# Performance work log

Hardware: AMD Instinct MI355X
Metric: run time of the kernel (lower is better)

Reference implementation:

```python
import jax, jax.numpy as jnp
import numpy as np

D_MODEL = 2048
N_HEADS = 16
D_K = D_MODEL // N_HEADS
NB_FEAT = 8  # ceil(ln(2048))
BLOCK_H = 1
BLOCK_W = 1
EPS = 1e-6


def setup_inputs() -> dict:
    key = jax.random.key(0)
    ks = jax.random.split(key, 8)
    B, S = 2, 4096
    q = jax.random.normal(ks[0], (B, S, D_MODEL), dtype=jnp.float32)
    k = jax.random.normal(ks[1], (B, S, D_MODEL), dtype=jnp.float32)
    v = jax.random.normal(ks[2], (B, S, D_MODEL), dtype=jnp.float32)
    # torch Linear weights [out, in]
    w_q = jax.random.normal(ks[3], (D_MODEL, D_MODEL), dtype=jnp.float32) / np.sqrt(D_MODEL)
    w_k = jax.random.normal(ks[4], (D_MODEL, D_MODEL), dtype=jnp.float32) / np.sqrt(D_MODEL)
    w_v = jax.random.normal(ks[5], (D_MODEL, D_MODEL), dtype=jnp.float32) / np.sqrt(D_MODEL)
    w_o = jax.random.normal(ks[6], (D_MODEL, D_MODEL), dtype=jnp.float32) / np.sqrt(D_MODEL)
    omega = jax.random.normal(ks[7], (NB_FEAT, D_K), dtype=jnp.float32) / np.sqrt(D_K)
    return {"q": q, "k": k, "v": v, "w_q": w_q, "w_k": w_k, "w_v": w_v, "w_o": w_o, "omega": omega}


def _kernel(x):
    # kernel_type == 'exp'
    return jnp.exp(-0.5 * x * x)


def reference(q, k, v, w_q, w_k, w_v, w_o, omega):
    B, Sq, D = q.shape
    Sk = k.shape[1]
    # projections (torch Linear: x @ W.T), split heads -> [B, S, H, d_k]
    qh = (q @ w_q.T).reshape(B, Sq, N_HEADS, D_K)
    kh = (k @ w_k.T).reshape(B, Sk, N_HEADS, D_K)
    vh = (v @ w_v.T).reshape(B, Sk, N_HEADS, D_K)
    # random-feature maps -> [B, S, H, nb]
    q_prime = _kernel(jnp.einsum('bshd,nd->bshn', qh, omega))
    k_prime = _kernel(jnp.einsum('bshd,nd->bshn', kh, omega))
    q_prime = q_prime / (q_prime.sum(-1, keepdims=True) + EPS)
    k_prime = k_prime / (k_prime.sum(-1, keepdims=True) + EPS)
    # causal prefix sums along sequence
    K_cum = jnp.cumsum(k_prime, axis=1)                                   # [B,S,H,nb]
    KV_cum = jnp.cumsum(k_prime[..., None] * vh[..., None, :], axis=1)    # [B,S,H,nb,d_k]
    # blockwise causal key selection
    q_idx = jnp.arange(Sq)
    key_idx = jnp.minimum((q_idx // BLOCK_H + 1) * BLOCK_W - 1, Sk - 1)   # [Sq]
    K_sel = K_cum[:, key_idx]    # [B,Sq,H,nb]
    KV_sel = KV_cum[:, key_idx]  # [B,Sq,H,nb,d_k]
    numerator = jnp.einsum('bshn,bshnd->bshd', q_prime, KV_sel)
    denominator = jnp.sum(q_prime * K_sel, axis=-1, keepdims=True)
    out = numerator / (denominator + EPS)
    out = out.reshape(B, Sq, D)
    return out @ w_o.T
```

## Files before the change

### kernel.cpp

```cpp
#include <hip/hip_runtime.h>
#include <hip/hip_bf16.h>
#include <cstdint>

#define B_SZ 2
#define S_LEN 4096
#define R_TOT 8192
#define DM 2048
#define NH 16
#define DK 128
#define NFEAT 8
#define CHUNK 128
#define NCHUNK 32
#define KSPL 512
#define EPSF 1e-6f

typedef short bf16x8_t __attribute__((ext_vector_type(8)));
typedef float f32x4_t __attribute__((ext_vector_type(4)));

__device__ __forceinline__ ushort f2bf(float f) {
  uint32_t u = __float_as_uint(f);
  u += 0x7FFF + ((u >> 16) & 1);
  return (ushort)(u >> 16);
}
__device__ __forceinline__ float bf2f(ushort u) {
  return __uint_as_float(((uint32_t)u) << 16);
}

__global__ __launch_bounds__(256) void prep_kernel(const float* __restrict__ v,
                                                   const float* __restrict__ w_v,
                                                   const float* __restrict__ w_o,
                                                   const float* __restrict__ w_q,
                                                   const float* __restrict__ w_k,
                                                   const float* __restrict__ omega,
                                                   ushort* __restrict__ xb,
                                                   ushort* __restrict__ wvb,
                                                   ushort* __restrict__ wob,
                                                   ushort* __restrict__ oqb,
                                                   ushort* __restrict__ okb) {
  const int bid = blockIdx.x;
  if (bid < 16384) {
    const int i = bid * 256 + threadIdx.x;
    float4 f = reinterpret_cast<const float4*>(v)[i];
    ushort4 o;
    o.x = f2bf(f.x); o.y = f2bf(f.y); o.z = f2bf(f.z); o.w = f2bf(f.w);
    reinterpret_cast<ushort4*>(xb)[i] = o;
  } else if (bid < 24576) {
    const int wb = bid - 16384;
    const float* src = (wb >= 4096) ? w_o : w_v;
    ushort* dst = (wb >= 4096) ? wob : wvb;
    const int i = (wb & 4095) * 256 + threadIdx.x;
    float4 f = reinterpret_cast<const float4*>(src)[i];
    ushort4 o;
    o.x = f2bf(f.x); o.y = f2bf(f.y); o.z = f2bf(f.z); o.w = f2bf(f.w);
    reinterpret_cast<ushort4*>(dst)[i] = o;
  } else {
    __shared__ float som[NFEAT * DK];
    const int fb = bid - 24576;
    const int z = fb >> 7, h = (fb >> 3) & 15, jb = fb & 7;
    const float* W = z ? w_k : w_q;
    ushort* O = z ? okb : oqb;
    const int j = jb * 256 + threadIdx.x;
    for (int i = threadIdx.x; i < NFEAT * DK; i += 256) som[i] = omega[i];
    __syncthreads();
    float acc[NFEAT] = {0.f, 0.f, 0.f, 0.f, 0.f, 0.f, 0.f, 0.f};
    for (int d = 0; d < DK; d++) {
      const float w = W[(size_t)(h * DK + d) * DM + j];
#pragma unroll
      for (int n = 0; n < NFEAT; n++) acc[n] += w * som[n * DK + d];
    }
#pragma unroll
    for (int n = 0; n < NFEAT; n++) O[(size_t)(h * NFEAT + n) * DM + j] = f2bf(acc[n]);
  }
}

#define MFMA_BLK(mb, A0_, A1_, A2_, A3_, B0_, B1_, B2_, B3_)                                  \
  acc[mb + 0][0] = __builtin_amdgcn_mfma_f32_16x16x32_bf16(A0_, B0_, acc[mb + 0][0], 0, 0, 0); \
  acc[mb + 1][0] = __builtin_amdgcn_mfma_f32_16x16x32_bf16(A1_, B0_, acc[mb + 1][0], 0, 0, 0); \
  acc[mb + 2][0] = __builtin_amdgcn_mfma_f32_16x16x32_bf16(A2_, B0_, acc[mb + 2][0], 0, 0, 0); \
  acc[mb + 3][0] = __builtin_amdgcn_mfma_f32_16x16x32_bf16(A3_, B0_, acc[mb + 3][0], 0, 0, 0); \
  acc[mb + 0][1] = __builtin_amdgcn_mfma_f32_16x16x32_bf16(A0_, B1_, acc[mb + 0][1], 0, 0, 0); \
  acc[mb + 1][1] = __builtin_amdgcn_mfma_f32_16x16x32_bf16(A1_, B1_, acc[mb + 1][1], 0, 0, 0); \
  acc[mb + 2][1] = __builtin_amdgcn_mfma_f32_16x16x32_bf16(A2_, B1_, acc[mb + 2][1], 0, 0, 0); \
  acc[mb + 3][1] = __builtin_amdgcn_mfma_f32_16x16x32_bf16(A3_, B1_, acc[mb + 3][1], 0, 0, 0); \
  acc[mb + 0][2] = __builtin_amdgcn_mfma_f32_16x16x32_bf16(A0_, B2_, acc[mb + 0][2], 0, 0, 0); \
  acc[mb + 1][2] = __builtin_amdgcn_mfma_f32_16x16x32_bf16(A1_, B2_, acc[mb + 1][2], 0, 0, 0); \
  acc[mb + 2][2] = __builtin_amdgcn_mfma_f32_16x16x32_bf16(A2_, B2_, acc[mb + 2][2], 0, 0, 0); \
  acc[mb + 3][2] = __builtin_amdgcn_mfma_f32_16x16x32_bf16(A3_, B2_, acc[mb + 3][2], 0, 0, 0); \
  acc[mb + 0][3] = __builtin_amdgcn_mfma_f32_16x16x32_bf16(A0_, B3_, acc[mb + 0][3], 0, 0, 0); \
  acc[mb + 1][3] = __builtin_amdgcn_mfma_f32_16x16x32_bf16(A1_, B3_, acc[mb + 1][3], 0, 0, 0); \
  acc[mb + 2][3] = __builtin_amdgcn_mfma_f32_16x16x32_bf16(A2_, B3_, acc[mb + 2][3], 0, 0, 0); \
  acc[mb + 3][3] = __builtin_amdgcn_mfma_f32_16x16x32_bf16(A3_, B3_, acc[mb + 3][3], 0, 0, 0);

template<int BF16OUT>
__global__ __launch_bounds__(512, 1) void gemm256(const ushort* __restrict__ A,
                                                  const ushort* __restrict__ Bm,
                                                  void* __restrict__ Cv,
                                                  int M, int N, int K) {
  __shared__ ushort lds[8 * 8192];
  const int tid = threadIdx.x;
  const int wave = tid >> 6, lane = tid & 63;
  const int wm = wave >> 2, wn = wave & 3;
  const int NKT = K >> 6;

  const int nb = N >> 8;
  const int cpx = gridDim.x >> 3;
  const int swz = (blockIdx.x & 7) * cpx + (blockIdx.x >> 3);
  const int bx = swz % nb, by = swz / nb;
  const int m0 = by * 256, n0 = bx * 256;

  auto stage = [&](int bufi, int ab, int kh, int kt, const ushort* G, int r0) {
    ushort* Lr = lds + (((bufi << 1) | ab) << 1 | kh) * 8192;
#pragma unroll
    for (int j = 0; j < 2; j++) {
      const int c = j * 512 + wave * 64 + lane;
      const int row = c >> 2, slot = c & 3;
      const int ss = slot ^ ((row >> 1) & 3);
      const ushort* g = G + (size_t)(r0 + row) * K + kt * 64 + kh * 32 + ss * 8;
      __builtin_amdgcn_global_load_lds(
          (const __attribute__((address_space(1))) void*)g,
          (__attribute__((address_space(3))) void*)(Lr + (j * 512 + wave * 64) * 8), 16, 0, 0);
    }
  };
  auto rdA = [&](int bufi, int kh, int m) -> bf16x8_t {
    const int row = wm * 128 + m * 16 + (lane & 15);
    const int slot = (lane >> 4) ^ ((row >> 1) & 3);
    return *reinterpret_cast<const bf16x8_t*>(lds + ((bufi << 2) | kh) * 8192 + row * 32 + slot * 8);
  };
  auto rdB = [&](int bufi, int kh, int nf) -> bf16x8_t {
    const int row = wn * 64 + nf * 16 + (lane & 15);
    const int slot = (lane >> 4) ^ ((row >> 1) & 3);
    return *reinterpret_cast<const bf16x8_t*>(lds + (((bufi << 1) | 1) << 1 | kh) * 8192 + row * 32 + slot * 8);
  };

  f32x4_t acc[8][4];
#pragma unroll
  for (int m = 0; m < 8; m++)
#pragma unroll
    for (int nf = 0; nf < 4; nf++) acc[m][nf] = (f32x4_t){0.f, 0.f, 0.f, 0.f};

  stage(0, 0, 0, 0, A, m0);  stage(0, 1, 0, 0, Bm, n0);
  stage(0, 0, 1, 0, A, m0);  stage(0, 1, 1, 0, Bm, n0);
  stage(1, 0, 0, 1, A, m0);  stage(1, 1, 0, 1, Bm, n0);
  asm volatile("s_waitcnt vmcnt(8)" ::: "memory");
  __builtin_amdgcn_s_barrier();
  __builtin_amdgcn_sched_barrier(0);

  bf16x8_t pA0 = rdA(0, 0, 0), pA1 = rdA(0, 0, 1), pA2 = rdA(0, 0, 2), pA3 = rdA(0, 0, 3);
  bf16x8_t B00 = rdB(0, 0, 0), B01 = rdB(0, 0, 1), B02 = rdB(0, 0, 2), B03 = rdB(0, 0, 3);
  bf16x8_t qA0, qA1, qA2, qA3, B10, B11, B12, B13;

  for (int t = 0; t < NKT; t++) {
    const int buf = t & 1;
    const int t1 = (t + 1 < NKT) ? t + 1 : NKT - 1;
    const int t2 = (t + 2 < NKT) ? t + 2 : NKT - 1;

    qA0 = rdA(buf, 0, 4); qA1 = rdA(buf, 0, 5); qA2 = rdA(buf, 0, 6); qA3 = rdA(buf, 0, 7);
    stage(buf ^ 1, 0, 1, t1, A, m0);
    __builtin_amdgcn_s_setprio(1);
    MFMA_BLK(0, pA0, pA1, pA2, pA3, B00, B01, B02, B03)
    __builtin_amdgcn_s_setprio(0);
    asm volatile("s_waitcnt vmcnt(6)" ::: "memory");
    __builtin_amdgcn_s_barrier();
    __builtin_amdgcn_sched_barrier(0);

    pA0 = rdA(buf, 1, 0); pA1 = rdA(buf, 1, 1); pA2 = rdA(buf, 1, 2); pA3 = rdA(buf, 1, 3);
    B10 = rdB(buf, 1, 0); B11 = rdB(buf, 1, 1); B12 = rdB(buf, 1, 2); B13 = rdB(buf, 1, 3);
    stage(buf ^ 1, 1, 1, t1, Bm, n0);
    __builtin_amdgcn_s_setprio(1);
    MFMA_BLK(4, qA0, qA1, qA2, qA3, B00, B01, B02, B03)
    __builtin_amdgcn_s_setprio(0);
    __builtin_amdgcn_s_barrier();
    __builtin_amdgcn_sched_barrier(0);

    qA0 = rdA(buf, 1, 4); qA1 = rdA(buf, 1, 5); qA2 = rdA(buf, 1, 6); qA3 = rdA(buf, 1, 7);
    stage(buf, 0, 0, t2, A, m0);
    __builtin_amdgcn_s_setprio(1);
    MFMA_BLK(0, pA0, pA1, pA2, pA3, B10, B11, B12, B13)
    __builtin_amdgcn_s_setprio(0);
    asm volatile("s_waitcnt vmcnt(6)" ::: "memory");
    __builtin_amdgcn_s_barrier();
    __builtin_amdgcn_sched_barrier(0);

    pA0 = rdA(buf ^ 1, 0, 0); pA1 = rdA(buf ^ 1, 0, 1); pA2 = rdA(buf ^ 1, 0, 2); pA3 = rdA(buf ^ 1, 0, 3);
    B00 = rdB(buf ^ 1, 0, 0); B01 = rdB(buf ^ 1, 0, 1); B02 = rdB(buf ^ 1, 0, 2); B03 = rdB(buf ^ 1, 0, 3);
    stage(buf, 1, 0, t2, Bm, n0);
    __builtin_amdgcn_s_setprio(1);
    MFMA_BLK(4, qA0, qA1, qA2, qA3, B10, B11, B12, B13)
    __builtin_amdgcn_s_setprio(0);
    __builtin_amdgcn_s_barrier();
    __builtin_amdgcn_sched_barrier(0);
  }
  asm volatile("s_waitcnt vmcnt(0)" ::: "memory");

#pragma unroll
  for (int m = 0; m < 8; m++) {
    const int rb = m0 + wm * 128 + m * 16 + (lane >> 4) * 4;
#pragma unroll
    for (int nf = 0; nf < 4; nf++) {
      const int col = n0 + wn * 64 + nf * 16 + (lane & 15);
#pragma unroll
      for (int r = 0; r < 4; r++) {
        const float val = acc[m][nf][r];
        if (BF16OUT)
          ((ushort*)Cv)[(size_t)(rb + r) * N + col] = f2bf(val);
        else
          ((float*)Cv)[(size_t)(rb + r) * N + col] = val;
      }
    }
  }
}

__global__ __launch_bounds__(256) void gemm_thin2(const float* __restrict__ qin,
                                                  const float* __restrict__ kin,
                                                  const ushort* __restrict__ oqb,
                                                  const ushort* __restrict__ okb,
                                                  float* __restrict__ P) {
  __shared__ ushort lds_a[128 * 32];
  __shared__ ushort lds_b[128 * 32];
  const int which = blockIdx.z;
  const float* A = which ? kin : qin;
  const ushort* Bm = which ? okb : oqb;
  const int t = threadIdx.x;
  const int wave = t >> 6, lane = t & 63;
  const int spl = blockIdx.x;
  const int m0 = blockIdx.y * 128;
  const int kb = spl * KSPL;
  const int wm = wave >> 1, wn = wave & 1;

  f32x4_t acc[4][4];
#pragma unroll
  for (int i = 0; i < 4; i++)
#pragma unroll
    for (int j = 0; j < 4; j++) acc[i][j] = (f32x4_t){0.f, 0.f, 0.f, 0.f};

  const int srow = lane >> 2;
  const int skoff = (lane & 3) * 8;

  for (int k0 = kb; k0 < kb + KSPL; k0 += 32) {
#pragma unroll
    for (int j = 0; j < 2; j++) {
      const int g = j * 256 + t;
      const int row = g >> 2, slot = g & 3;
      const float4* gp = reinterpret_cast<const float4*>(A + (size_t)(m0 + row) * DM + k0 + slot * 8);
      const float4 f0 = gp[0], f1 = gp[1];
      union { ushort u[8]; bf16x8_t v; } pk;
      pk.u[0] = f2bf(f0.x); pk.u[1] = f2bf(f0.y); pk.u[2] = f2bf(f0.z); pk.u[3] = f2bf(f0.w);
      pk.u[4] = f2bf(f1.x); pk.u[5] = f2bf(f1.y); pk.u[6] = f2bf(f1.z); pk.u[7] = f2bf(f1.w);
      *reinterpret_cast<bf16x8_t*>(lds_a + row * 32 + slot * 8) = pk.v;
    }
#pragma unroll
    for (int i = 0; i < 2; i++) {
      const int rgrp = i * 4 + wave;
      const int row = rgrp * 16 + srow;
      const ushort* gb = Bm + (size_t)row * DM + (k0 + skoff);
      __builtin_amdgcn_global_load_lds(
          (const __attribute__((address_space(1))) void*)gb,
          (__attribute__((address_space(3))) void*)(lds_b + rgrp * 512), 16, 0, 0);
    }
    __syncthreads();
    bf16x8_t af[4], bfr[4];
#pragma unroll
    for (int i = 0; i < 4; i++) {
      af[i]  = *reinterpret_cast<const bf16x8_t*>(
          lds_a + (wm * 64 + i * 16 + (lane & 15)) * 32 + (lane >> 4) * 8);
      bfr[i] = *reinterpret_cast<const bf16x8_t*>(
          lds_b + (wn * 64 + i * 16 + (lane & 15)) * 32 + (lane >> 4) * 8);
    }
#pragma unroll
    for (int i = 0; i < 4; i++)
#pragma unroll
      for (int j = 0; j < 4; j++)
        acc[i][j] = __builtin_amdgcn_mfma_f32_16x16x32_bf16(af[i], bfr[j], acc[i][j], 0, 0, 0);
    __syncthreads();
  }

  float* Pp = P + (size_t)which * (4ull * R_TOT * 128) + (size_t)spl * ((size_t)R_TOT * 128);
#pragma unroll
  for (int i = 0; i < 4; i++) {
    const int rb = m0 + wm * 64 + i * 16 + (lane >> 4) * 4;
#pragma unroll
    for (int j = 0; j < 4; j++) {
      const int col = wn * 64 + j * 16 + (lane & 15);
#pragma unroll
      for (int r = 0; r < 4; r++)
        Pp[(size_t)(rb + r) * 128 + col] = acc[i][j][r];
    }
  }
}

__global__ __launch_bounds__(256) void feat2x2(const float* __restrict__ P,
                                               float* __restrict__ qf,
                                               float* __restrict__ kf) {
  const int which = blockIdx.y;
  const float* Pb = P + (size_t)which * (4ull * R_TOT * 128);
  float* F = which ? kf : qf;
  const int g = blockIdx.x * 256 + threadIdx.x;
  const int row = g >> 4, h = g & 15;
  float4 a = {0.f, 0.f, 0.f, 0.f}, c = {0.f, 0.f, 0.f, 0.f};
#pragma unroll
  for (int s = 0; s < 4; s++) {
    const float4* xp = reinterpret_cast<const float4*>(
        Pb + (size_t)s * ((size_t)R_TOT * 128) + (size_t)row * 128 + h * NFEAT);
    const float4 u = xp[0], w = xp[1];
    a.x += u.x; a.y += u.y; a.z += u.z; a.w += u.w;
    c.x += w.x; c.y += w.y; c.z += w.z; c.w += w.w;
  }
  float x[8] = {a.x, a.y, a.z, a.w, c.x, c.y, c.z, c.w};
  float f[8], s = 0.f;
#pragma unroll
  for (int n = 0; n < 8; n++) { f[n] = __expf(-0.5f * x[n] * x[n]); s += f[n]; }
  const float inv = 1.f / (s + EPSF);
  const int b = row >> 12, sidx = row & 4095;
  float* out = F + ((size_t)(h * 2 + b) * 4096 + sidx) * 8;
  float4 o0 = {f[0] * inv, f[1] * inv, f[2] * inv, f[3] * inv};
  float4 o1 = {f[4] * inv, f[5] * inv, f[6] * inv, f[7] * inv};
  reinterpret_cast<float4*>(out)[0] = o0;
  reinterpret_cast<float4*>(out)[1] = o1;
}

__global__ __launch_bounds__(128) void chunk_sum_kernel(const float* __restrict__ KF,
                                                        const ushort* __restrict__ VH,
                                                        float* __restrict__ CKV,
                                                        float* __restrict__ CK) {
  const int cid = blockIdx.x;
  const int c = cid & 31, bh = cid >> 5, b = bh >> 4, h = bh & 15;
  const int d = threadIdx.x;
  __shared__ float s_kf[CHUNK * 8];
  const size_t fbase = ((size_t)(h * 2 + b) * 4096 + (size_t)c * CHUNK) * 8;
  {
    float4 a0 = *reinterpret_cast<const float4*>(KF + fbase + d * 8);
    float4 a1 = *reinterpret_cast<const float4*>(KF + fbase + d * 8 + 4);
    *reinterpret_cast<float4*>(s_kf + d * 8) = a0;
    *reinterpret_cast<float4*>(s_kf + d * 8 + 4) = a1;
  }
  __syncthreads();
  float kv[8] = {0, 0, 0, 0, 0, 0, 0, 0};
  float ks = 0.f;
  const ushort* vp = VH + ((size_t)b * S_LEN + (size_t)c * CHUNK) * DM + h * DK + d;
  for (int s = 0; s < CHUNK; s++) {
    const float v = bf2f(vp[(size_t)s * DM]);
#pragma unroll
    for (int n = 0; n < 8; n++) kv[n] += s_kf[s * 8 + n] * v;
    ks += s_kf[s * 8 + (d & 7)];
  }
#pragma unroll
  for (int n = 0; n < 8; n++) CKV[((size_t)cid * 8 + n) * 128 + d] = kv[n];
  if (d < 8) CK[cid * 8 + d] = ks;
}

__global__ __launch_bounds__(128) void chunk_scan2(float* __restrict__ CKV,
                                                   float* __restrict__ CK) {
  const int bh = blockIdx.x >> 3, n = blockIdx.x & 7;
  const int d = threadIdx.x;
  float v[NCHUNK];
#pragma unroll
  for (int c = 0; c < NCHUNK; c++)
    v[c] = CKV[((size_t)(bh * NCHUNK + c) * 8 + n) * 128 + d];
  float run = 0.f;
#pragma unroll
  for (int c = 0; c < NCHUNK; c++) {
    const float tv = v[c];
    CKV[((size_t)(bh * NCHUNK + c) * 8 + n) * 128 + d] = run;
    run += tv;
  }
  if (d < 32) {
    const int i = (bh * NCHUNK + d) * 8 + n;
    const float orig = CK[i];
    float inc = orig;
#pragma unroll
    for (int off = 1; off < 32; off <<= 1) {
      const float o = __shfl_up(inc, off, 32);
      if (d >= off) inc += o;
    }
    CK[i] = inc - orig;
  }
}

__global__ __launch_bounds__(128) void attn_scan_kernel(const float* __restrict__ QF,
                                                        const float* __restrict__ KF,
                                                        const ushort* __restrict__ VH,
                                                        const float* __restrict__ CKV,
                                                        const float* __restrict__ CK,
                                                        ushort* __restrict__ AO) {
  const int cid = blockIdx.x;
  const int c = cid & 31, bh = cid >> 5, b = bh >> 4, h = bh & 15;
  const int d = threadIdx.x;
  __shared__ float s_qf[CHUNK * 8];
  __shared__ float s_kf[CHUNK * 8];
  const size_t fbase = ((size_t)(h * 2 + b) * 4096 + (size_t)c * CHUNK) * 8;
  {
    float4 a0 = *reinterpret_cast<const float4*>(QF + fbase + d * 8);
    float4 a1 = *reinterpret_cast<const float4*>(QF + fbase + d * 8 + 4);
    float4 b0 = *reinterpret_cast<const float4*>(KF + fbase + d * 8);
    float4 b1 = *reinterpret_cast<const float4*>(KF + fbase + d * 8 + 4);
    *reinterpret_cast<float4*>(s_qf + d * 8) = a0;
    *reinterpret_cast<float4*>(s_qf + d * 8 + 4) = a1;
    *reinterpret_cast<float4*>(s_kf + d * 8) = b0;
    *reinterpret_cast<float4*>(s_kf + d * 8 + 4) = b1;
  }
  float kv[8], krun[8];
#pragma unroll
  for (int n = 0; n < 8; n++) kv[n] = CKV[((size_t)cid * 8 + n) * 128 + d];
#pragma unroll
  for (int n = 0; n < 8; n++) krun[n] = CK[cid * 8 + n];
  __syncthreads();
  const size_t row0 = (size_t)b * S_LEN + (size_t)c * CHUNK;
  const ushort* vp = VH + row0 * DM + h * DK + d;
  ushort* op = AO + row0 * DM + h * DK + d;
  for (int s = 0; s < CHUNK; s++) {
    const float v = bf2f(vp[(size_t)s * DM]);
    float num = 0.f, den = 0.f;
#pragma unroll
    for (int n = 0; n < 8; n++) {
      const float kf = s_kf[s * 8 + n];
      kv[n] += kf * v;
      krun[n] += kf;
      const float qf = s_qf[s * 8 + n];
      num += qf * kv[n];
      den += qf * krun[n];
    }
    op[(size_t)s * DM] = f2bf(num / (den + EPSF));
  }
}

extern "C" void kernel_launch(void* const* d_in, const int* in_sizes, int n_in,
                              void* d_out, int out_size, void* d_ws, size_t ws_size,
                              hipStream_t stream) {
  const float* q     = (const float*)d_in[0];
  const float* k     = (const float*)d_in[1];
  const float* v     = (const float*)d_in[2];
  const float* w_q   = (const float*)d_in[3];
  const float* w_k   = (const float*)d_in[4];
  const float* w_v   = (const float*)d_in[5];
  const float* w_o   = (const float*)d_in[6];
  const float* omega = (const float*)d_in[7];

  char* ws = (char*)d_ws;
  const size_t DD2 = (size_t)DM * DM * 2;
  const size_t OD2 = (size_t)NH * NFEAT * DM * 2;
  const size_t RD2 = (size_t)R_TOT * DM * 2;
  const size_t X4  = (size_t)R_TOT * NH * NFEAT * 4;

  ushort* wvb = (ushort*)(ws);
  ushort* wob = (ushort*)(ws + DD2);
  ushort* oqb = (ushort*)(ws + 2 * DD2);
  ushort* okb = (ushort*)(ws + 2 * DD2 + OD2);
  ushort* xb  = (ushort*)(ws + 2 * DD2 + 2 * OD2);
  ushort* vhb = (ushort*)(ws + 2 * DD2 + 2 * OD2 + RD2);
  float*  xp4 = (float*) (ws + 2 * DD2 + 2 * OD2 + RD2);
  float*  qf  = (float*) (ws + 2 * DD2 + 2 * OD2 + 2 * RD2);
  float*  kf  = (float*) (ws + 2 * DD2 + 2 * OD2 + 2 * RD2 + X4);
  float*  ckv = (float*) (ws + 2 * DD2 + 2 * OD2 + 2 * RD2 + 2 * X4);
  float*  ck  = (float*) (ws + 2 * DD2 + 2 * OD2 + 2 * RD2 + 3 * X4);
  ushort* ao  = xb;

  prep_kernel<<<dim3(24832), 256, 0, stream>>>(v, w_v, w_o, w_q, w_k, omega,
                                               xb, wvb, wob, oqb, okb);

  gemm_thin2<<<dim3(DM / KSPL, R_TOT / 128, 2), 256, 0, stream>>>(q, k, oqb, okb, xp4);
  feat2x2<<<dim3(R_TOT * NH / 256, 2), 256, 0, stream>>>(xp4, qf, kf);

  gemm256<1><<<dim3((R_TOT / 256) * (DM / 256)), 512, 0, stream>>>(xb, wvb, (void*)vhb, R_TOT, DM, DM);

  chunk_sum_kernel<<<dim3(B_SZ * NH * NCHUNK), 128, 0, stream>>>(kf, vhb, ckv, ck);
  chunk_scan2<<<dim3(B_SZ * NH * 8), 128, 0, stream>>>(ckv, ck);
  attn_scan_kernel<<<dim3(B_SZ * NH * NCHUNK), 128, 0, stream>>>(qf, kf, vhb, ckv, ck, ao);

  gemm256<0><<<dim3((R_TOT / 256) * (DM / 256)), 512, 0, stream>>>(ao, wob, d_out, R_TOT, DM, DM);
}
```

Before: 290.4 us.

## Move v-to-bf16 cast into thin GEMM launch and drop sched barriers

The cast of the v input to bf16 moves out of the prep kernel and into the thin q/k feature-projection GEMM launch as extra blocks (grid x grows from 4 to 132). The bandwidth-bound cast can then run alongside the compute-bound thin GEMM blocks instead of in a separate serialized phase. Separately, the sched_barrier calls after each s_barrier in the main bf16 GEMM are removed, which lets the compiler reorder LDS reads across phase boundaries but may break the hand-tuned instruction interleaving.

```diff
diff --git a/kernel.cpp b/kernel.cpp
--- a/kernel.cpp
+++ b/kernel.cpp
@@ -26,36 +26,27 @@
   return __uint_as_float(((uint32_t)u) << 16);
 }
 
-__global__ __launch_bounds__(256) void prep_kernel(const float* __restrict__ v,
-                                                   const float* __restrict__ w_v,
+__global__ __launch_bounds__(256) void prep_kernel(const float* __restrict__ w_v,
                                                    const float* __restrict__ w_o,
                                                    const float* __restrict__ w_q,
                                                    const float* __restrict__ w_k,
                                                    const float* __restrict__ omega,
-                                                   ushort* __restrict__ xb,
                                                    ushort* __restrict__ wvb,
                                                    ushort* __restrict__ wob,
                                                    ushort* __restrict__ oqb,
                                                    ushort* __restrict__ okb) {
   const int bid = blockIdx.x;
-  if (bid < 16384) {
-    const int i = bid * 256 + threadIdx.x;
-    float4 f = reinterpret_cast<const float4*>(v)[i];
-    ushort4 o;
-    o.x = f2bf(f.x); o.y = f2bf(f.y); o.z = f2bf(f.z); o.w = f2bf(f.w);
-    reinterpret_cast<ushort4*>(xb)[i] = o;
-  } else if (bid < 24576) {
-    const int wb = bid - 16384;
-    const float* src = (wb >= 4096) ? w_o : w_v;
-    ushort* dst = (wb >= 4096) ? wob : wvb;
-    const int i = (wb & 4095) * 256 + threadIdx.x;
+  if (bid < 8192) {
+    const float* src = (bid >= 4096) ? w_o : w_v;
+    ushort* dst = (bid >= 4096) ? wob : wvb;
+    const int i = (bid & 4095) * 256 + threadIdx.x;
     float4 f = reinterpret_cast<const float4*>(src)[i];
     ushort4 o;
     o.x = f2bf(f.x); o.y = f2bf(f.y); o.z = f2bf(f.z); o.w = f2bf(f.w);
     reinterpret_cast<ushort4*>(dst)[i] = o;
   } else {
     __shared__ float som[NFEAT * DK];
-    const int fb = bid - 24576;
+    const int fb = bid - 8192;
     const int z = fb >> 7, h = (fb >> 3) & 15, jb = fb & 7;
     const float* W = z ? w_k : w_q;
     ushort* O = z ? okb : oqb;
@@ -143,7 +134,6 @@
   stage(1, 0, 0, 1, A, m0);  stage(1, 1, 0, 1, Bm, n0);
   asm volatile("s_waitcnt vmcnt(8)" ::: "memory");
   __builtin_amdgcn_s_barrier();
-  __builtin_amdgcn_sched_barrier(0);
 
   bf16x8_t pA0 = rdA(0, 0, 0), pA1 = rdA(0, 0, 1), pA2 = rdA(0, 0, 2), pA3 = rdA(0, 0, 3);
   bf16x8_t B00 = rdB(0, 0, 0), B01 = rdB(0, 0, 1), B02 = rdB(0, 0, 2), B03 = rdB(0, 0, 3);
@@ -161,7 +151,6 @@
     __builtin_amdgcn_s_setprio(0);
     asm volatile("s_waitcnt vmcnt(6)" ::: "memory");
     __builtin_amdgcn_s_barrier();
-    __builtin_amdgcn_sched_barrier(0);
 
     pA0 = rdA(buf, 1, 0); pA1 = rdA(buf, 1, 1); pA2 = rdA(buf, 1, 2); pA3 = rdA(buf, 1, 3);
     B10 = rdB(buf, 1, 0); B11 = rdB(buf, 1, 1); B12 = rdB(buf, 1, 2); B13 = rdB(buf, 1, 3);
@@ -170,7 +159,6 @@
     MFMA_BLK(4, qA0, qA1, qA2, qA3, B00, B01, B02, B03)
     __builtin_amdgcn_s_setprio(0);
     __builtin_amdgcn_s_barrier();
-    __builtin_amdgcn_sched_barrier(0);
 
     qA0 = rdA(buf, 1, 4); qA1 = rdA(buf, 1, 5); qA2 = rdA(buf, 1, 6); qA3 = rdA(buf, 1, 7);
     stage(buf, 0, 0, t2, A, m0);
@@ -179,7 +167,6 @@
     __builtin_amdgcn_s_setprio(0);
     asm volatile("s_waitcnt vmcnt(6)" ::: "memory");
     __builtin_amdgcn_s_barrier();
-    __builtin_amdgcn_sched_barrier(0);
 
     pA0 = rdA(buf ^ 1, 0, 0); pA1 = rdA(buf ^ 1, 0, 1); pA2 = rdA(buf ^ 1, 0, 2); pA3 = rdA(buf ^ 1, 0, 3);
     B00 = rdB(buf ^ 1, 0, 0); B01 = rdB(buf ^ 1, 0, 1); B02 = rdB(buf ^ 1, 0, 2); B03 = rdB(buf ^ 1, 0, 3);
@@ -188,7 +175,6 @@
     MFMA_BLK(4, qA0, qA1, qA2, qA3, B10, B11, B12, B13)
     __builtin_amdgcn_s_setprio(0);
     __builtin_amdgcn_s_barrier();
-    __builtin_amdgcn_sched_barrier(0);
   }
   asm volatile("s_waitcnt vmcnt(0)" ::: "memory");
 
@@ -210,17 +196,30 @@
   }
 }
 
-__global__ __launch_bounds__(256) void gemm_thin2(const float* __restrict__ qin,
-                                                  const float* __restrict__ kin,
-                                                  const ushort* __restrict__ oqb,
-                                                  const ushort* __restrict__ okb,
-                                                  float* __restrict__ P) {
+__global__ __launch_bounds__(256) void thin_cast(const float* __restrict__ qin,
+                                                 const float* __restrict__ kin,
+                                                 const float* __restrict__ vin,
+                                                 const ushort* __restrict__ oqb,
+                                                 const ushort* __restrict__ okb,
+                                                 float* __restrict__ P,
+                                                 ushort* __restrict__ xb) {
   __shared__ ushort lds_a[128 * 32];
   __shared__ ushort lds_b[128 * 32];
+  const int t = threadIdx.x;
+
+  if (blockIdx.x >= 4) {
+    const int cast_bid = (blockIdx.x - 4) * 128 + blockIdx.y * 2 + blockIdx.z;
+    const int i = cast_bid * 256 + t;
+    float4 f = reinterpret_cast<const float4*>(vin)[i];
+    ushort4 o;
+    o.x = f2bf(f.x); o.y = f2bf(f.y); o.z = f2bf(f.z); o.w = f2bf(f.w);
+    reinterpret_cast<ushort4*>(xb)[i] = o;
+    return;
+  }
+
   const int which = blockIdx.z;
   const float* A = which ? kin : qin;
   const ushort* Bm = which ? okb : oqb;
-  const int t = threadIdx.x;
   const int wave = t >> 6, lane = t & 63;
   const int spl = blockIdx.x;
   const int m0 = blockIdx.y * 128;
@@ -454,10 +453,10 @@
   float*  ck  = (float*) (ws + 2 * DD2 + 2 * OD2 + 2 * RD2 + 3 * X4);
   ushort* ao  = xb;
 
-  prep_kernel<<<dim3(24832), 256, 0, stream>>>(v, w_v, w_o, w_q, w_k, omega,
-                                               xb, wvb, wob, oqb, okb);
-
-  gemm_thin2<<<dim3(DM / KSPL, R_TOT / 128, 2), 256, 0, stream>>>(q, k, oqb, okb, xp4);
+  prep_kernel<<<dim3(8448), 256, 0, stream>>>(w_v, w_o, w_q, w_k, omega,
+                                              wvb, wob, oqb, okb);
+
+  thin_cast<<<dim3(132, 64, 2), 256, 0, stream>>>(q, k, v, oqb, okb, xp4, xb);
   feat2x2<<<dim3(R_TOT * NH / 256, 2), 256, 0, stream>>>(xp4, qf, kf);
 
   gemm256<1><<<dim3((R_TOT / 256) * (DM / 256)), 512, 0, stream>>>(xb, wvb, (void*)vhb, R_TOT, DM, DM);
```

New measurement: 306.8 us. 5.6% more time.
